# Kernel optimization log

Measured on AMD Instinct MI355X. Metric: run time of the kernel, lower is better.

The kernel has to match this reference:

```python
import jax, jax.numpy as jnp
import numpy as np

N = 40000          # nodes
E = 640000         # edges (before self-loops)
G = 64             # graphs
EMBED_DIM = 128
GAT_HIDDEN = 64    # per-head channels for g1/g2
GAT_OUT_DIM = 64   # per-head channels for g3 (concat=False)
HEADS = (4, 4, 4)
NEG_SLOPE = 0.2


def setup_inputs() -> dict:
    key = jax.random.key(0)
    ks = jax.random.split(key, 16)
    x = jax.random.normal(ks[0], (N, EMBED_DIM), dtype=jnp.float32)
    edge_index = jax.random.randint(ks[1], (2, E), 0, N, dtype=jnp.int64)
    batch = jnp.sort(jax.random.randint(ks[2], (N,), 0, G, dtype=jnp.int64))

    def lin(k, i, o):
        return jax.random.normal(k, (i, o), dtype=jnp.float32) * (1.0 / np.sqrt(i))

    H1, H2, H3 = HEADS
    d1_in, d1_out = EMBED_DIM, GAT_HIDDEN
    d2_in, d2_out = GAT_HIDDEN * H1, GAT_HIDDEN
    d3_in, d3_out = GAT_HIDDEN * H2, GAT_OUT_DIM
    params = dict(
        Wl1=lin(ks[3], d1_in, H1 * d1_out), Wr1=lin(ks[4], d1_in, H1 * d1_out),
        att1=jax.random.normal(ks[5], (H1, d1_out), dtype=jnp.float32) * 0.1,
        b1=jnp.zeros((H1 * d1_out,), jnp.float32),
        Wl2=lin(ks[6], d2_in, H2 * d2_out), Wr2=lin(ks[7], d2_in, H2 * d2_out),
        att2=jax.random.normal(ks[8], (H2, d2_out), dtype=jnp.float32) * 0.1,
        b2=jnp.zeros((H2 * d2_out,), jnp.float32),
        Wl3=lin(ks[9], d3_in, H3 * d3_out), Wr3=lin(ks[10], d3_in, H3 * d3_out),
        att3=jax.random.normal(ks[11], (H3, d3_out), dtype=jnp.float32) * 0.1,
        b3=jnp.zeros((d3_out,), jnp.float32),
        Wc=lin(ks[12], GAT_OUT_DIM, 2), bc=jnp.zeros((2,), jnp.float32),
    )
    return dict(x=x, edge_index=edge_index, batch=batch, **params)


def _gatv2(x, src, dst, Wl, Wr, att, bias, heads, out_c, concat):
    n = x.shape[0]
    xl = (x @ Wl).reshape(n, heads, out_c)   # source transform
    xr = (x @ Wr).reshape(n, heads, out_c)   # target transform
    # per-edge GATv2 score: att . LeakyReLU(xl[j] + xr[i])
    e = jax.nn.leaky_relu(xl[src] + xr[dst], NEG_SLOPE)      # [E,H,C]
    score = jnp.einsum('ehc,hc->eh', e, att)                  # [E,H]
    # segment softmax over incoming edges of each target node
    smax = jax.ops.segment_max(score, dst, num_segments=n)
    escore = jnp.exp(score - smax[dst])
    denom = jax.ops.segment_sum(escore, dst, num_segments=n)
    alpha = escore / (denom[dst] + 1e-16)                     # [E,H]
    out = jax.ops.segment_sum(alpha[:, :, None] * xl[src], dst, num_segments=n)
    out = out.reshape(n, heads * out_c) if concat else out.mean(axis=1)
    return out + bias


def reference(x, edge_index, batch, Wl1, Wr1, att1, b1, Wl2, Wr2, att2, b2,
              Wl3, Wr3, att3, b3, Wc, bc):
    n = x.shape[0]
    loops = jnp.arange(n, dtype=edge_index.dtype)
    src = jnp.concatenate([edge_index[0], loops])  # add self-loops (PyG default)
    dst = jnp.concatenate([edge_index[1], loops])
    act = lambda h: jax.nn.leaky_relu(h, NEG_SLOPE)
    h = act(_gatv2(x, src, dst, Wl1, Wr1, att1, b1, HEADS[0], GAT_HIDDEN, True))
    h = act(_gatv2(h, src, dst, Wl2, Wr2, att2, b2, HEADS[1], GAT_HIDDEN, True))
    h = _gatv2(h, src, dst, Wl3, Wr3, att3, b3, HEADS[2], GAT_OUT_DIM, False)
    g = jax.ops.segment_max(h, batch, num_segments=G)  # global_max_pool
    logits = g @ Wc + bc
    return logits, g
```

## Files before the change

kernel.cpp:

```cpp
#include <hip/hip_runtime.h>
#include <cstdint>

#define NN 40000
#define EE 640000
#define GG 64

typedef short bf16x8 __attribute__((ext_vector_type(8)));
typedef float f32x4 __attribute__((ext_vector_type(4)));

__device__ __forceinline__ float lrelu(float x) { return x > 0.f ? x : 0.2f * x; }

__device__ __forceinline__ unsigned short f2bf(float f) {
    unsigned u = __float_as_uint(f);
    return (unsigned short)((u + 0x7FFFu + ((u >> 16) & 1u)) >> 16);
}
__device__ __forceinline__ float bf2f(unsigned short h) {
    return __uint_as_float(((unsigned)h) << 16);
}

__device__ __forceinline__ unsigned fenc(float x) {
    unsigned u = __float_as_uint(x);
    return (u & 0x80000000u) ? ~u : (u | 0x80000000u);
}
__device__ __forceinline__ float fdec(unsigned e) {
    unsigned u = (e & 0x80000000u) ? (e ^ 0x80000000u) : ~e;
    return __uint_as_float(u);
}
#define ENC_NEG_INF 0x007FFFFFu

__global__ void k_init(int* deg, unsigned* gmax) {
    int i = blockIdx.x * blockDim.x + threadIdx.x;
    if (i < NN) deg[i] = 0;
    if (i < GG * 64) gmax[i] = ENC_NEG_INF;
}

__global__ void k_count(const int* __restrict__ dst, int* deg) {
    int e = blockIdx.x * blockDim.x + threadIdx.x;
    if (e < EE) atomicAdd(&deg[dst[e]], 1);
}

#define SCAN_T 1024
__global__ __launch_bounds__(SCAN_T) void k_scan(const int* __restrict__ deg,
                                                 int* row_ptr, int* cursor) {
    __shared__ int part[SCAN_T];
    const int t = threadIdx.x;
    const int CH = (NN + SCAN_T - 1) / SCAN_T;
    const int base = t * CH;
    int s = 0;
    for (int j = 0; j < CH; ++j) {
        int idx = base + j;
        if (idx < NN) s += deg[idx];
    }
    part[t] = s;
    __syncthreads();
    for (int off = 1; off < SCAN_T; off <<= 1) {
        int v = (t >= off) ? part[t - off] : 0;
        __syncthreads();
        part[t] += v;
        __syncthreads();
    }
    int run = (t == 0) ? 0 : part[t - 1];
    for (int j = 0; j < CH; ++j) {
        int idx = base + j;
        if (idx < NN) {
            row_ptr[idx] = run;
            cursor[idx]  = run;
            run += deg[idx];
        }
    }
    if (t == SCAN_T - 1) row_ptr[NN] = run;
}

__global__ void k_scatter(const int* __restrict__ src, const int* __restrict__ dst,
                          int* cursor, int* csr_src) {
    int e = blockIdx.x * blockDim.x + threadIdx.x;
    if (e < EE) {
        int p = atomicAdd(&cursor[dst[e]], 1);
        csr_src[p] = src[e];
    }
}

__global__ void k_xsplit(const float* __restrict__ x,
                         ushort* __restrict__ ah, ushort* __restrict__ am,
                         ushort* __restrict__ al, int total4) {
    int i = blockIdx.x * blockDim.x + threadIdx.x;
    if (i >= total4) return;
    float4 v = ((const float4*)x)[i];
    ushort4 H, M, L;
    float* pv = &v.x;
    unsigned short* pH = &H.x; unsigned short* pM = &M.x; unsigned short* pL = &L.x;
#pragma unroll
    for (int j = 0; j < 4; ++j) {
        float a = pv[j];
        unsigned short h = f2bf(a);
        float r1 = a - bf2f(h);
        unsigned short m = f2bf(r1);
        float r2 = r1 - bf2f(m);
        unsigned short l = f2bf(r2);
        pH[j] = h; pM[j] = m; pL[j] = l;
    }
    ((ushort4*)ah)[i] = H;
    ((ushort4*)am)[i] = M;
    ((ushort4*)al)[i] = L;
}

__global__ __launch_bounds__(256) void k_wsplit(const float* __restrict__ W, int K,
                                                ushort* __restrict__ th,
                                                ushort* __restrict__ tm,
                                                ushort* __restrict__ tl) {
    __shared__ float t[32][33];
    const int n0 = blockIdx.x * 32;
    const int k0 = blockIdx.y * 32;
    const int tx = threadIdx.x;
    const int ty = threadIdx.y;
#pragma unroll
    for (int i = 0; i < 4; ++i) {
        int kl = ty * 4 + i;
        t[kl][tx] = W[(size_t)(k0 + kl) * 256 + n0 + tx];
    }
    __syncthreads();
#pragma unroll
    for (int i = 0; i < 4; ++i) {
        int nl = ty * 4 + i;
        float a = t[tx][nl];
        unsigned short h = f2bf(a);
        float r1 = a - bf2f(h);
        unsigned short m = f2bf(r1);
        float r2 = r1 - bf2f(m);
        unsigned short l = f2bf(r2);
        size_t o = (size_t)(n0 + nl) * K + k0 + tx;
        th[o] = h; tm[o] = m; tl[o] = l;
    }
}

#define GBM 128
#define GBK 32
__global__ __launch_bounds__(256, 2) void gemm3(const ushort* __restrict__ Ah,
                                                const ushort* __restrict__ Am,
                                                const ushort* __restrict__ Al,
                                                const ushort* __restrict__ Bh,
                                                const ushort* __restrict__ Bm,
                                                const ushort* __restrict__ Bl,
                                                float* __restrict__ C,
                                                int M, int K) {
    __shared__ ushort sA[3][GBM * GBK];
    __shared__ ushort sB[3][GBM * GBK];
    const int tid  = threadIdx.x;
    const int lane = tid & 63;
    const int wv   = tid >> 6;
    const int wm   = wv & 1;
    const int wn   = wv >> 1;
    const int bm   = blockIdx.x * GBM;
    const int bn   = blockIdx.y * 128;

    f32x4 acc[4][4];
#pragma unroll
    for (int i = 0; i < 4; ++i)
#pragma unroll
        for (int j = 0; j < 4; ++j)
            acc[i][j] = (f32x4){0.f, 0.f, 0.f, 0.f};

    const ushort* Aarr[3] = {Ah, Am, Al};
    const ushort* Barr[3] = {Bh, Bm, Bl};

    for (int k0 = 0; k0 < K; k0 += GBK) {
#pragma unroll
        for (int qq = 0; qq < 2; ++qq) {
            const int q   = tid + qq * 256;
            const int row = q >> 2;
            const int c   = q & 3;
            const int cs  = c ^ ((row >> 1) & 3);
            const int lidx = row * 32 + cs * 8;
            int ga = bm + row; if (ga >= M) ga = M - 1;
            const size_t aoff = (size_t)ga * K + k0 + c * 8;
            const size_t boff = (size_t)(bn + row) * K + k0 + c * 8;
#pragma unroll
            for (int s = 0; s < 3; ++s) {
                *(uint4*)&sA[s][lidx] = *(const uint4*)&Aarr[s][aoff];
                *(uint4*)&sB[s][lidx] = *(const uint4*)&Barr[s][boff];
            }
        }
        __syncthreads();

        bf16x8 a[3][4], b[3][4];
        const int fc = lane >> 4;
        const int fr = lane & 15;
#pragma unroll
        for (int mi = 0; mi < 4; ++mi) {
            const int row = wm * 64 + mi * 16 + fr;
            const int cs  = fc ^ ((row >> 1) & 3);
            const int idx = row * 32 + cs * 8;
#pragma unroll
            for (int s = 0; s < 3; ++s)
                a[s][mi] = *(const bf16x8*)&sA[s][idx];
        }
#pragma unroll
        for (int ni = 0; ni < 4; ++ni) {
            const int row = wn * 64 + ni * 16 + fr;
            const int cs  = fc ^ ((row >> 1) & 3);
            const int idx = row * 32 + cs * 8;
#pragma unroll
            for (int s = 0; s < 3; ++s)
                b[s][ni] = *(const bf16x8*)&sB[s][idx];
        }

#pragma unroll
        for (int mi = 0; mi < 4; ++mi)
#pragma unroll
            for (int ni = 0; ni < 4; ++ni) {
                f32x4 c0 = acc[mi][ni];
                c0 = __builtin_amdgcn_mfma_f32_16x16x32_bf16(a[0][mi], b[0][ni], c0, 0, 0, 0);
                c0 = __builtin_amdgcn_mfma_f32_16x16x32_bf16(a[0][mi], b[1][ni], c0, 0, 0, 0);
                c0 = __builtin_amdgcn_mfma_f32_16x16x32_bf16(a[1][mi], b[0][ni], c0, 0, 0, 0);
                c0 = __builtin_amdgcn_mfma_f32_16x16x32_bf16(a[0][mi], b[2][ni], c0, 0, 0, 0);
                c0 = __builtin_amdgcn_mfma_f32_16x16x32_bf16(a[2][mi], b[0][ni], c0, 0, 0, 0);
                c0 = __builtin_amdgcn_mfma_f32_16x16x32_bf16(a[1][mi], b[1][ni], c0, 0, 0, 0);
                acc[mi][ni] = c0;
            }
        __syncthreads();
    }

#pragma unroll
    for (int mi = 0; mi < 4; ++mi) {
#pragma unroll
        for (int r = 0; r < 4; ++r) {
            const int row = bm + wm * 64 + mi * 16 + (lane >> 4) * 4 + r;
            if (row < M) {
#pragma unroll
                for (int ni = 0; ni < 4; ++ni) {
                    const int col = bn + wn * 64 + ni * 16 + (lane & 15);
                    C[(size_t)row * 256 + col] = acc[mi][ni][r];
                }
            }
        }
    }
}

template <int MODE>
__global__ __launch_bounds__(256) void k_aggregate(const float* __restrict__ xl,
                                                   const float* __restrict__ xr,
                                                   const float* __restrict__ att,
                                                   const float* __restrict__ bias,
                                                   const int* __restrict__ row_ptr,
                                                   const int* __restrict__ csr_src,
                                                   ushort* __restrict__ oh,
                                                   ushort* __restrict__ om,
                                                   ushort* __restrict__ ol,
                                                   float* __restrict__ of) {
    const int wave = threadIdx.x >> 6;
    const int lane = threadIdx.x & 63;
    const int node = blockIdx.x * 4 + wave;
    if (node >= NN) return;

    const float4 xri = ((const float4*)(xr + (size_t)node * 256))[lane];
    const float4 av  = ((const float4*)att)[lane];

    float m = -INFINITY, d = 0.f;
    float acc0 = 0.f, acc1 = 0.f, acc2 = 0.f, acc3 = 0.f;

    const int start = row_ptr[node];
    const int end   = row_ptr[node + 1];
    const int L = end - start + 1;

    int i = 0;
    for (; i + 1 < L; i += 2) {
        const int ea = start + i, eb = start + i + 1;
        const int sa = (ea < end) ? csr_src[ea] : node;
        const int sb = (eb < end) ? csr_src[eb] : node;
        const float4 xa = ((const float4*)(xl + (size_t)sa * 256))[lane];
        const float4 xb = ((const float4*)(xl + (size_t)sb * 256))[lane];
        float pa = av.x * lrelu(xa.x + xri.x) + av.y * lrelu(xa.y + xri.y)
                 + av.z * lrelu(xa.z + xri.z) + av.w * lrelu(xa.w + xri.w);
        float pb = av.x * lrelu(xb.x + xri.x) + av.y * lrelu(xb.y + xri.y)
                 + av.z * lrelu(xb.z + xri.z) + av.w * lrelu(xb.w + xri.w);
        pa += __shfl_xor(pa, 1); pb += __shfl_xor(pb, 1);
        pa += __shfl_xor(pa, 2); pb += __shfl_xor(pb, 2);
        pa += __shfl_xor(pa, 4); pb += __shfl_xor(pb, 4);
        pa += __shfl_xor(pa, 8); pb += __shfl_xor(pb, 8);

        const float mn    = fmaxf(m, fmaxf(pa, pb));
        const float scale = __expf(m - mn);
        const float fa    = __expf(pa - mn);
        const float fb    = __expf(pb - mn);
        d    = d * scale + fa + fb;
        acc0 = acc0 * scale + fa * xa.x + fb * xb.x;
        acc1 = acc1 * scale + fa * xa.y + fb * xb.y;
        acc2 = acc2 * scale + fa * xa.z + fb * xb.z;
        acc3 = acc3 * scale + fa * xa.w + fb * xb.w;
        m = mn;
    }
    if (i < L) {
        const int ea = start + i;
        const int sa = (ea < end) ? csr_src[ea] : node;
        const float4 xa = ((const float4*)(xl + (size_t)sa * 256))[lane];
        float pa = av.x * lrelu(xa.x + xri.x) + av.y * lrelu(xa.y + xri.y)
                 + av.z * lrelu(xa.z + xri.z) + av.w * lrelu(xa.w + xri.w);
        pa += __shfl_xor(pa, 1);
        pa += __shfl_xor(pa, 2);
        pa += __shfl_xor(pa, 4);
        pa += __shfl_xor(pa, 8);
        const float mn    = fmaxf(m, pa);
        const float scale = __expf(m - mn);
        const float fa    = __expf(pa - mn);
        d    = d * scale + fa;
        acc0 = acc0 * scale + fa * xa.x;
        acc1 = acc1 * scale + fa * xa.y;
        acc2 = acc2 * scale + fa * xa.z;
        acc3 = acc3 * scale + fa * xa.w;
        m = mn;
    }

    const float inv = 1.f / (d + 1e-16f);
    if (MODE == 0) {
        const int c = lane * 4;
        float v[4];
        v[0] = lrelu(acc0 * inv + bias[c + 0]);
        v[1] = lrelu(acc1 * inv + bias[c + 1]);
        v[2] = lrelu(acc2 * inv + bias[c + 2]);
        v[3] = lrelu(acc3 * inv + bias[c + 3]);
        ushort4 H, M4, L4;
        unsigned short* pH = &H.x; unsigned short* pM = &M4.x; unsigned short* pL = &L4.x;
#pragma unroll
        for (int j = 0; j < 4; ++j) {
            unsigned short h = f2bf(v[j]);
            float r1 = v[j] - bf2f(h);
            unsigned short mm = f2bf(r1);
            float r2 = r1 - bf2f(mm);
            pH[j] = h; pM[j] = mm; pL[j] = f2bf(r2);
        }
        const size_t o = (size_t)node * 64 + lane;
        ((ushort4*)oh)[o] = H;
        ((ushort4*)om)[o] = M4;
        ((ushort4*)ol)[o] = L4;
    } else {
        float v0 = acc0 * inv, v1 = acc1 * inv, v2 = acc2 * inv, v3 = acc3 * inv;
        v0 += __shfl_xor(v0, 16); v0 += __shfl_xor(v0, 32);
        v1 += __shfl_xor(v1, 16); v1 += __shfl_xor(v1, 32);
        v2 += __shfl_xor(v2, 16); v2 += __shfl_xor(v2, 32);
        v3 += __shfl_xor(v3, 16); v3 += __shfl_xor(v3, 32);
        if (lane < 16) {
            const int c = lane * 4;
            float4 o;
            o.x = v0 * 0.25f + bias[c + 0];
            o.y = v1 * 0.25f + bias[c + 1];
            o.z = v2 * 0.25f + bias[c + 2];
            o.w = v3 * 0.25f + bias[c + 3];
            ((float4*)(of + (size_t)node * 64))[lane] = o;
        }
    }
}

#define PNB 32
__global__ __launch_bounds__(64) void k_pool(const float* __restrict__ h3,
                                             const int* __restrict__ batch,
                                             unsigned* gmax) {
    const int lane = threadIdx.x;
    const int start = blockIdx.x * PNB;
    if (start >= NN) return;
    const int end = min(start + PNB, NN);
    int curg = batch[start];
    float best = -INFINITY;
    for (int n = start; n < end; ++n) {
        int g = batch[n];
        if (g != curg) {
            atomicMax(&gmax[curg * 64 + lane], fenc(best));
            best = -INFINITY;
            curg = g;
        }
        best = fmaxf(best, h3[(size_t)n * 64 + lane]);
    }
    atomicMax(&gmax[curg * 64 + lane], fenc(best));
}

__global__ void k_decode(const unsigned* __restrict__ gmax, float* __restrict__ outg) {
    int i = blockIdx.x * blockDim.x + threadIdx.x;
    if (i < GG * 64) outg[i] = fdec(gmax[i]);
}

__global__ __launch_bounds__(128) void k_head(const float* __restrict__ g,
                                              const float* __restrict__ Wc,
                                              const float* __restrict__ bc,
                                              float* __restrict__ logits) {
    const int t = threadIdx.x;
    const int gr = t >> 1, o = t & 1;
    float s = bc[o];
    for (int c = 0; c < 64; ++c) s = fmaf(g[gr * 64 + c], Wc[c * 2 + o], s);
    logits[t] = s;
}

extern "C" void kernel_launch(void* const* d_in, const int* in_sizes, int n_in,
                              void* d_out, int out_size, void* d_ws, size_t ws_size,
                              hipStream_t stream) {
    const float* x     = (const float*)d_in[0];
    const int*   ei    = (const int*)d_in[1];
    const int*   batch = (const int*)d_in[2];
    const float* Wl1 = (const float*)d_in[3];
    const float* Wr1 = (const float*)d_in[4];
    const float* att1 = (const float*)d_in[5];
    const float* b1  = (const float*)d_in[6];
    const float* Wl2 = (const float*)d_in[7];
    const float* Wr2 = (const float*)d_in[8];
    const float* att2 = (const float*)d_in[9];
    const float* b2  = (const float*)d_in[10];
    const float* Wl3 = (const float*)d_in[11];
    const float* Wr3 = (const float*)d_in[12];
    const float* att3 = (const float*)d_in[13];
    const float* b3  = (const float*)d_in[14];
    const float* Wc  = (const float*)d_in[15];
    const float* bc  = (const float*)d_in[16];
    float* out = (float*)d_out;

    char* ws = (char*)d_ws;
    size_t off = 0;
    auto alloc = [&](size_t bytes) -> void* {
        void* p = ws + off;
        off += (bytes + 255) & ~(size_t)255;
        return p;
    };
    float*  xlout = (float*)alloc((size_t)NN * 256 * 4);
    float*  xrout = (float*)alloc((size_t)NN * 256 * 4);
    ushort* Ah    = (ushort*)alloc((size_t)NN * 256 * 2);
    ushort* Am    = (ushort*)alloc((size_t)NN * 256 * 2);
    ushort* Al    = (ushort*)alloc((size_t)NN * 256 * 2);
    ushort* wt[6][3];
    for (int w = 0; w < 6; ++w)
        for (int s = 0; s < 3; ++s)
            wt[w][s] = (ushort*)alloc((size_t)256 * 256 * 2);
    int*   deg     = (int*)alloc((size_t)NN * 4);
    int*   cursor  = (int*)alloc((size_t)NN * 4);
    int*   row_ptr = (int*)alloc((size_t)(NN + 1) * 4);
    int*   csr_src = (int*)alloc((size_t)EE * 4);
    unsigned* gmax = (unsigned*)alloc((size_t)GG * 64 * 4);
    float* h3 = (float*)Ah;
    if (off > ws_size) return;

    const int* esrc = ei;
    const int* edst = ei + EE;

    k_init<<<(NN + 255) / 256, 256, 0, stream>>>(deg, gmax);
    k_count<<<(EE + 255) / 256, 256, 0, stream>>>(edst, deg);
    k_scan<<<1, SCAN_T, 0, stream>>>(deg, row_ptr, cursor);
    k_scatter<<<(EE + 255) / 256, 256, 0, stream>>>(esrc, edst, cursor, csr_src);

    k_xsplit<<<(NN * 128 / 4 + 255) / 256, 256, 0, stream>>>(x, Ah, Am, Al, NN * 128 / 4);
    const float* Ws[6] = {Wl1, Wr1, Wl2, Wr2, Wl3, Wr3};
    const int    Ks[6] = {128, 128, 256, 256, 256, 256};
    for (int w = 0; w < 6; ++w) {
        dim3 g(8, Ks[w] / 32), b(32, 8);
        k_wsplit<<<g, b, 0, stream>>>(Ws[w], Ks[w], wt[w][0], wt[w][1], wt[w][2]);
    }

    const dim3 gg((NN + GBM - 1) / GBM, 2);
    const int agg_blocks = NN / 4;

    gemm3<<<gg, 256, 0, stream>>>(Ah, Am, Al, wt[0][0], wt[0][1], wt[0][2], xlout, NN, 128);
    gemm3<<<gg, 256, 0, stream>>>(Ah, Am, Al, wt[1][0], wt[1][1], wt[1][2], xrout, NN, 128);
    k_aggregate<0><<<agg_blocks, 256, 0, stream>>>(xlout, xrout, att1, b1, row_ptr, csr_src,
                                                   Ah, Am, Al, nullptr);
    gemm3<<<gg, 256, 0, stream>>>(Ah, Am, Al, wt[2][0], wt[2][1], wt[2][2], xlout, NN, 256);
    gemm3<<<gg, 256, 0, stream>>>(Ah, Am, Al, wt[3][0], wt[3][1], wt[3][2], xrout, NN, 256);
    k_aggregate<0><<<agg_blocks, 256, 0, stream>>>(xlout, xrout, att2, b2, row_ptr, csr_src,
                                                   Ah, Am, Al, nullptr);
    gemm3<<<gg, 256, 0, stream>>>(Ah, Am, Al, wt[4][0], wt[4][1], wt[4][2], xlout, NN, 256);
    gemm3<<<gg, 256, 0, stream>>>(Ah, Am, Al, wt[5][0], wt[5][1], wt[5][2], xrout, NN, 256);
    k_aggregate<1><<<agg_blocks, 256, 0, stream>>>(xlout, xrout, att3, b3, row_ptr, csr_src,
                                                   nullptr, nullptr, nullptr, h3);

    k_pool<<<(NN + PNB - 1) / PNB, 64, 0, stream>>>(h3, batch, gmax);
    k_decode<<<(GG * 64 + 255) / 256, 256, 0, stream>>>(gmax, out + 128);
    k_head<<<1, 128, 0, stream>>>(out + 128, Wc, bc, out);
}
```

Baseline: 805.9 us.

## Use 2-term bf16 split GEMM, direct-to-LDS loads, and lazy-rescale softmax aggregation

The fp32-emulating GEMM drops from a three-way bf16 split (six MFMAs per tile) to a two-way split (three MFMAs), and the low-part arrays, their writes and their storage are removed. Global-to-LDS staging now uses the global_load_lds builtin, with each wave loading one operand. The aggregation loop processes four edges per iteration and skips the online-softmax rescale unless a score exceeds the running max by more than 8. These changes cut GEMM compute and memory traffic, register pressure and exp work, at the cost of lower GEMM precision (about 16 mantissa bits).

```diff
diff --git a/kernel.cpp b/kernel.cpp
--- a/kernel.cpp
+++ b/kernel.cpp
@@ -27,6 +27,13 @@
     return __uint_as_float(u);
 }
 #define ENC_NEG_INF 0x007FFFFFu
+
+__device__ __forceinline__ void gload16(const void* g, void* l) {
+    __builtin_amdgcn_global_load_lds(
+        (const __attribute__((address_space(1))) unsigned int*)g,
+        (__attribute__((address_space(3))) unsigned int*)l,
+        16, 0, 0);
+}
 
 __global__ void k_init(int* deg, unsigned* gmax) {
     int i = blockIdx.x * blockDim.x + threadIdx.x;
@@ -81,33 +88,27 @@
 }
 
 __global__ void k_xsplit(const float* __restrict__ x,
-                         ushort* __restrict__ ah, ushort* __restrict__ am,
-                         ushort* __restrict__ al, int total4) {
+                         ushort* __restrict__ ah, ushort* __restrict__ am, int total4) {
     int i = blockIdx.x * blockDim.x + threadIdx.x;
     if (i >= total4) return;
     float4 v = ((const float4*)x)[i];
-    ushort4 H, M, L;
+    ushort4 H, M;
     float* pv = &v.x;
-    unsigned short* pH = &H.x; unsigned short* pM = &M.x; unsigned short* pL = &L.x;
+    unsigned short* pH = &H.x; unsigned short* pM = &M.x;
 #pragma unroll
     for (int j = 0; j < 4; ++j) {
         float a = pv[j];
         unsigned short h = f2bf(a);
-        float r1 = a - bf2f(h);
-        unsigned short m = f2bf(r1);
-        float r2 = r1 - bf2f(m);
-        unsigned short l = f2bf(r2);
-        pH[j] = h; pM[j] = m; pL[j] = l;
+        pH[j] = h;
+        pM[j] = f2bf(a - bf2f(h));
     }
     ((ushort4*)ah)[i] = H;
     ((ushort4*)am)[i] = M;
-    ((ushort4*)al)[i] = L;
 }
 
 __global__ __launch_bounds__(256) void k_wsplit(const float* __restrict__ W, int K,
                                                 ushort* __restrict__ th,
-                                                ushort* __restrict__ tm,
-                                                ushort* __restrict__ tl) {
+                                                ushort* __restrict__ tm) {
     __shared__ float t[32][33];
     const int n0 = blockIdx.x * 32;
     const int k0 = blockIdx.y * 32;
@@ -124,27 +125,24 @@
         int nl = ty * 4 + i;
         float a = t[tx][nl];
         unsigned short h = f2bf(a);
-        float r1 = a - bf2f(h);
-        unsigned short m = f2bf(r1);
-        float r2 = r1 - bf2f(m);
-        unsigned short l = f2bf(r2);
         size_t o = (size_t)(n0 + nl) * K + k0 + tx;
-        th[o] = h; tm[o] = m; tl[o] = l;
+        th[o] = h;
+        tm[o] = f2bf(a - bf2f(h));
     }
 }
 
 #define GBM 128
 #define GBK 32
-__global__ __launch_bounds__(256, 2) void gemm3(const ushort* __restrict__ Ah,
+__global__ __launch_bounds__(256, 2) void gemm2(const ushort* __restrict__ Ah,
                                                 const ushort* __restrict__ Am,
-                                                const ushort* __restrict__ Al,
                                                 const ushort* __restrict__ Bh,
                                                 const ushort* __restrict__ Bm,
-                                                const ushort* __restrict__ Bl,
                                                 float* __restrict__ C,
                                                 int M, int K) {
-    __shared__ ushort sA[3][GBM * GBK];
-    __shared__ ushort sB[3][GBM * GBK];
+    __shared__ ushort sAh[GBM * GBK];
+    __shared__ ushort sAm[GBM * GBK];
+    __shared__ ushort sBh[GBM * GBK];
+    __shared__ ushort sBm[GBM * GBK];
     const int tid  = threadIdx.x;
     const int lane = tid & 63;
     const int wv   = tid >> 6;
@@ -153,6 +151,10 @@
     const int bm   = blockIdx.x * GBM;
     const int bn   = blockIdx.y * 128;
 
+    const ushort* gsrc = (wv == 0) ? Ah : (wv == 1) ? Am : (wv == 2) ? Bh : Bm;
+    ushort* lbase = (wv == 0) ? sAh : (wv == 1) ? sAm : (wv == 2) ? sBh : sBm;
+    const int rowbase = (wv < 2) ? bm : bn;
+
     f32x4 acc[4][4];
 #pragma unroll
     for (int i = 0; i < 4; ++i)
@@ -160,48 +162,36 @@
         for (int j = 0; j < 4; ++j)
             acc[i][j] = (f32x4){0.f, 0.f, 0.f, 0.f};
 
-    const ushort* Aarr[3] = {Ah, Am, Al};
-    const ushort* Barr[3] = {Bh, Bm, Bl};
+    const int rl = lane >> 2;
+    const int cs = lane & 3;
+    const int fc = lane >> 4;
+    const int fr = lane & 15;
 
     for (int k0 = 0; k0 < K; k0 += GBK) {
 #pragma unroll
-        for (int qq = 0; qq < 2; ++qq) {
-            const int q   = tid + qq * 256;
-            const int row = q >> 2;
-            const int c   = q & 3;
-            const int cs  = c ^ ((row >> 1) & 3);
-            const int lidx = row * 32 + cs * 8;
-            int ga = bm + row; if (ga >= M) ga = M - 1;
-            const size_t aoff = (size_t)ga * K + k0 + c * 8;
-            const size_t boff = (size_t)(bn + row) * K + k0 + c * 8;
-#pragma unroll
-            for (int s = 0; s < 3; ++s) {
-                *(uint4*)&sA[s][lidx] = *(const uint4*)&Aarr[s][aoff];
-                *(uint4*)&sB[s][lidx] = *(const uint4*)&Barr[s][boff];
-            }
+        for (int j = 0; j < 8; ++j) {
+            const int lrow = j * 16 + rl;
+            const int c    = cs ^ ((lrow >> 1) & 3);
+            int grow = rowbase + lrow;
+            grow = (grow >= M) ? (M - 1) : grow;
+            gload16(gsrc + (size_t)grow * K + k0 + c * 8, lbase + j * 512);
         }
         __syncthreads();
 
-        bf16x8 a[3][4], b[3][4];
-        const int fc = lane >> 4;
-        const int fr = lane & 15;
+        bf16x8 aH[4], aM[4], bH[4], bM[4];
 #pragma unroll
         for (int mi = 0; mi < 4; ++mi) {
             const int row = wm * 64 + mi * 16 + fr;
-            const int cs  = fc ^ ((row >> 1) & 3);
-            const int idx = row * 32 + cs * 8;
-#pragma unroll
-            for (int s = 0; s < 3; ++s)
-                a[s][mi] = *(const bf16x8*)&sA[s][idx];
+            const int idx = row * 32 + (fc ^ ((row >> 1) & 3)) * 8;
+            aH[mi] = *(const bf16x8*)&sAh[idx];
+            aM[mi] = *(const bf16x8*)&sAm[idx];
         }
 #pragma unroll
         for (int ni = 0; ni < 4; ++ni) {
             const int row = wn * 64 + ni * 16 + fr;
-            const int cs  = fc ^ ((row >> 1) & 3);
-            const int idx = row * 32 + cs * 8;
-#pragma unroll
-            for (int s = 0; s < 3; ++s)
-                b[s][ni] = *(const bf16x8*)&sB[s][idx];
+            const int idx = row * 32 + (fc ^ ((row >> 1) & 3)) * 8;
+            bH[ni] = *(const bf16x8*)&sBh[idx];
+            bM[ni] = *(const bf16x8*)&sBm[idx];
         }
 
 #pragma unroll
@@ -209,12 +199,9 @@
 #pragma unroll
             for (int ni = 0; ni < 4; ++ni) {
                 f32x4 c0 = acc[mi][ni];
-                c0 = __builtin_amdgcn_mfma_f32_16x16x32_bf16(a[0][mi], b[0][ni], c0, 0, 0, 0);
-                c0 = __builtin_amdgcn_mfma_f32_16x16x32_bf16(a[0][mi], b[1][ni], c0, 0, 0, 0);
-                c0 = __builtin_amdgcn_mfma_f32_16x16x32_bf16(a[1][mi], b[0][ni], c0, 0, 0, 0);
-                c0 = __builtin_amdgcn_mfma_f32_16x16x32_bf16(a[0][mi], b[2][ni], c0, 0, 0, 0);
-                c0 = __builtin_amdgcn_mfma_f32_16x16x32_bf16(a[2][mi], b[0][ni], c0, 0, 0, 0);
-                c0 = __builtin_amdgcn_mfma_f32_16x16x32_bf16(a[1][mi], b[1][ni], c0, 0, 0, 0);
+                c0 = __builtin_amdgcn_mfma_f32_16x16x32_bf16(aH[mi], bH[ni], c0, 0, 0, 0);
+                c0 = __builtin_amdgcn_mfma_f32_16x16x32_bf16(aH[mi], bM[ni], c0, 0, 0, 0);
+                c0 = __builtin_amdgcn_mfma_f32_16x16x32_bf16(aM[mi], bH[ni], c0, 0, 0, 0);
                 acc[mi][ni] = c0;
             }
         __syncthreads();
@@ -245,7 +232,6 @@
                                                    const int* __restrict__ csr_src,
                                                    ushort* __restrict__ oh,
                                                    ushort* __restrict__ om,
-                                                   ushort* __restrict__ ol,
                                                    float* __restrict__ of) {
     const int wave = threadIdx.x >> 6;
     const int lane = threadIdx.x & 63;
@@ -256,84 +242,109 @@
     const float4 av  = ((const float4*)att)[lane];
 
     float m = -INFINITY, d = 0.f;
-    float acc0 = 0.f, acc1 = 0.f, acc2 = 0.f, acc3 = 0.f;
+    float a0 = 0.f, a1 = 0.f, a2 = 0.f, a3 = 0.f;
 
     const int start = row_ptr[node];
-    const int end   = row_ptr[node + 1];
-    const int L = end - start + 1;
+    const int endp  = row_ptr[node + 1];
+    const int L = endp - start + 1;
 
     int i = 0;
-    for (; i + 1 < L; i += 2) {
-        const int ea = start + i, eb = start + i + 1;
-        const int sa = (ea < end) ? csr_src[ea] : node;
-        const int sb = (eb < end) ? csr_src[eb] : node;
-        const float4 xa = ((const float4*)(xl + (size_t)sa * 256))[lane];
-        const float4 xb = ((const float4*)(xl + (size_t)sb * 256))[lane];
-        float pa = av.x * lrelu(xa.x + xri.x) + av.y * lrelu(xa.y + xri.y)
-                 + av.z * lrelu(xa.z + xri.z) + av.w * lrelu(xa.w + xri.w);
-        float pb = av.x * lrelu(xb.x + xri.x) + av.y * lrelu(xb.y + xri.y)
-                 + av.z * lrelu(xb.z + xri.z) + av.w * lrelu(xb.w + xri.w);
-        pa += __shfl_xor(pa, 1); pb += __shfl_xor(pb, 1);
-        pa += __shfl_xor(pa, 2); pb += __shfl_xor(pb, 2);
-        pa += __shfl_xor(pa, 4); pb += __shfl_xor(pb, 4);
-        pa += __shfl_xor(pa, 8); pb += __shfl_xor(pb, 8);
-
-        const float mn    = fmaxf(m, fmaxf(pa, pb));
-        const float scale = __expf(m - mn);
-        const float fa    = __expf(pa - mn);
-        const float fb    = __expf(pb - mn);
-        d    = d * scale + fa + fb;
-        acc0 = acc0 * scale + fa * xa.x + fb * xb.x;
-        acc1 = acc1 * scale + fa * xa.y + fb * xb.y;
-        acc2 = acc2 * scale + fa * xa.z + fb * xb.z;
-        acc3 = acc3 * scale + fa * xa.w + fb * xb.w;
-        m = mn;
-    }
-    if (i < L) {
-        const int ea = start + i;
-        const int sa = (ea < end) ? csr_src[ea] : node;
-        const float4 xa = ((const float4*)(xl + (size_t)sa * 256))[lane];
-        float pa = av.x * lrelu(xa.x + xri.x) + av.y * lrelu(xa.y + xri.y)
-                 + av.z * lrelu(xa.z + xri.z) + av.w * lrelu(xa.w + xri.w);
-        pa += __shfl_xor(pa, 1);
-        pa += __shfl_xor(pa, 2);
-        pa += __shfl_xor(pa, 4);
-        pa += __shfl_xor(pa, 8);
-        const float mn    = fmaxf(m, pa);
-        const float scale = __expf(m - mn);
-        const float fa    = __expf(pa - mn);
-        d    = d * scale + fa;
-        acc0 = acc0 * scale + fa * xa.x;
-        acc1 = acc1 * scale + fa * xa.y;
-        acc2 = acc2 * scale + fa * xa.z;
-        acc3 = acc3 * scale + fa * xa.w;
-        m = mn;
+    for (; i + 4 <= L; i += 4) {
+        const int e0 = start + i;
+        const int s0 = (e0     < endp) ? csr_src[e0]     : node;
+        const int s1 = (e0 + 1 < endp) ? csr_src[e0 + 1] : node;
+        const int s2 = (e0 + 2 < endp) ? csr_src[e0 + 2] : node;
+        const int s3 = (e0 + 3 < endp) ? csr_src[e0 + 3] : node;
+        const float4 x0 = ((const float4*)(xl + (size_t)s0 * 256))[lane];
+        const float4 x1 = ((const float4*)(xl + (size_t)s1 * 256))[lane];
+        const float4 x2 = ((const float4*)(xl + (size_t)s2 * 256))[lane];
+        const float4 x3 = ((const float4*)(xl + (size_t)s3 * 256))[lane];
+        float p0 = av.x * lrelu(x0.x + xri.x) + av.y * lrelu(x0.y + xri.y)
+                 + av.z * lrelu(x0.z + xri.z) + av.w * lrelu(x0.w + xri.w);
+        float p1 = av.x * lrelu(x1.x + xri.x) + av.y * lrelu(x1.y + xri.y)
+                 + av.z * lrelu(x1.z + xri.z) + av.w * lrelu(x1.w + xri.w);
+        float p2 = av.x * lrelu(x2.x + xri.x) + av.y * lrelu(x2.y + xri.y)
+                 + av.z * lrelu(x2.z + xri.z) + av.w * lrelu(x2.w + xri.w);
+        float p3 = av.x * lrelu(x3.x + xri.x) + av.y * lrelu(x3.y + xri.y)
+                 + av.z * lrelu(x3.z + xri.z) + av.w * lrelu(x3.w + xri.w);
+        p0 += __shfl_xor(p0, 1); p1 += __shfl_xor(p1, 1);
+        p2 += __shfl_xor(p2, 1); p3 += __shfl_xor(p3, 1);
+        p0 += __shfl_xor(p0, 2); p1 += __shfl_xor(p1, 2);
+        p2 += __shfl_xor(p2, 2); p3 += __shfl_xor(p3, 2);
+        p0 += __shfl_xor(p0, 4); p1 += __shfl_xor(p1, 4);
+        p2 += __shfl_xor(p2, 4); p3 += __shfl_xor(p3, 4);
+        p0 += __shfl_xor(p0, 8); p1 += __shfl_xor(p1, 8);
+        p2 += __shfl_xor(p2, 8); p3 += __shfl_xor(p3, 8);
+
+        const float pm = fmaxf(fmaxf(p0, p1), fmaxf(p2, p3));
+        if (__all(pm <= m + 8.f)) {
+            const float f0 = __expf(p0 - m), f1 = __expf(p1 - m);
+            const float f2 = __expf(p2 - m), f3 = __expf(p3 - m);
+            d  += f0 + f1 + f2 + f3;
+            a0 += f0 * x0.x + f1 * x1.x + f2 * x2.x + f3 * x3.x;
+            a1 += f0 * x0.y + f1 * x1.y + f2 * x2.y + f3 * x3.y;
+            a2 += f0 * x0.z + f1 * x1.z + f2 * x2.z + f3 * x3.z;
+            a3 += f0 * x0.w + f1 * x1.w + f2 * x2.w + f3 * x3.w;
+        } else {
+            const float mn = fmaxf(m, pm);
+            const float sc = __expf(m - mn);
+            const float f0 = __expf(p0 - mn), f1 = __expf(p1 - mn);
+            const float f2 = __expf(p2 - mn), f3 = __expf(p3 - mn);
+            d  = d  * sc + f0 + f1 + f2 + f3;
+            a0 = a0 * sc + f0 * x0.x + f1 * x1.x + f2 * x2.x + f3 * x3.x;
+            a1 = a1 * sc + f0 * x0.y + f1 * x1.y + f2 * x2.y + f3 * x3.y;
+            a2 = a2 * sc + f0 * x0.z + f1 * x1.z + f2 * x2.z + f3 * x3.z;
+            a3 = a3 * sc + f0 * x0.w + f1 * x1.w + f2 * x2.w + f3 * x3.w;
+            m = mn;
+        }
+    }
+    for (; i < L; ++i) {
+        const int e0 = start + i;
+        const int s0 = (e0 < endp) ? csr_src[e0] : node;
+        const float4 x0 = ((const float4*)(xl + (size_t)s0 * 256))[lane];
+        float p0 = av.x * lrelu(x0.x + xri.x) + av.y * lrelu(x0.y + xri.y)
+                 + av.z * lrelu(x0.z + xri.z) + av.w * lrelu(x0.w + xri.w);
+        p0 += __shfl_xor(p0, 1);
+        p0 += __shfl_xor(p0, 2);
+        p0 += __shfl_xor(p0, 4);
+        p0 += __shfl_xor(p0, 8);
+        if (__all(p0 <= m + 8.f)) {
+            const float f0 = __expf(p0 - m);
+            d += f0; a0 += f0 * x0.x; a1 += f0 * x0.y; a2 += f0 * x0.z; a3 += f0 * x0.w;
+        } else {
+            const float mn = fmaxf(m, p0);
+            const float sc = __expf(m - mn);
+            const float f0 = __expf(p0 - mn);
+            d  = d  * sc + f0;
+            a0 = a0 * sc + f0 * x0.x;
+            a1 = a1 * sc + f0 * x0.y;
+            a2 = a2 * sc + f0 * x0.z;
+            a3 = a3 * sc + f0 * x0.w;
+            m = mn;
+        }
     }
 
     const float inv = 1.f / (d + 1e-16f);
     if (MODE == 0) {
         const int c = lane * 4;
         float v[4];
-        v[0] = lrelu(acc0 * inv + bias[c + 0]);
-        v[1] = lrelu(acc1 * inv + bias[c + 1]);
-        v[2] = lrelu(acc2 * inv + bias[c + 2]);
-        v[3] = lrelu(acc3 * inv + bias[c + 3]);
-        ushort4 H, M4, L4;
-        unsigned short* pH = &H.x; unsigned short* pM = &M4.x; unsigned short* pL = &L4.x;
+        v[0] = lrelu(a0 * inv + bias[c + 0]);
+        v[1] = lrelu(a1 * inv + bias[c + 1]);
+        v[2] = lrelu(a2 * inv + bias[c + 2]);
+        v[3] = lrelu(a3 * inv + bias[c + 3]);
+        ushort4 H, M4;
+        unsigned short* pH = &H.x; unsigned short* pM = &M4.x;
 #pragma unroll
         for (int j = 0; j < 4; ++j) {
             unsigned short h = f2bf(v[j]);
-            float r1 = v[j] - bf2f(h);
-            unsigned short mm = f2bf(r1);
-            float r2 = r1 - bf2f(mm);
-            pH[j] = h; pM[j] = mm; pL[j] = f2bf(r2);
+            pH[j] = h;
+            pM[j] = f2bf(v[j] - bf2f(h));
         }
         const size_t o = (size_t)node * 64 + lane;
         ((ushort4*)oh)[o] = H;
         ((ushort4*)om)[o] = M4;
-        ((ushort4*)ol)[o] = L4;
     } else {
-        float v0 = acc0 * inv, v1 = acc1 * inv, v2 = acc2 * inv, v3 = acc3 * inv;
+        float v0 = a0 * inv, v1 = a1 * inv, v2 = a2 * inv, v3 = a3 * inv;
         v0 += __shfl_xor(v0, 16); v0 += __shfl_xor(v0, 32);
         v1 += __shfl_xor(v1, 16); v1 += __shfl_xor(v1, 32);
         v2 += __shfl_xor(v2, 16); v2 += __shfl_xor(v2, 32);
@@ -421,10 +432,9 @@
     float*  xrout = (float*)alloc((size_t)NN * 256 * 4);
     ushort* Ah    = (ushort*)alloc((size_t)NN * 256 * 2);
     ushort* Am    = (ushort*)alloc((size_t)NN * 256 * 2);
-    ushort* Al    = (ushort*)alloc((size_t)NN * 256 * 2);
-    ushort* wt[6][3];
+    ushort* wt[6][2];
     for (int w = 0; w < 6; ++w)
-        for (int s = 0; s < 3; ++s)
+        for (int s = 0; s < 2; ++s)
             wt[w][s] = (ushort*)alloc((size_t)256 * 256 * 2);
     int*   deg     = (int*)alloc((size_t)NN * 4);
     int*   cursor  = (int*)alloc((size_t)NN * 4);
@@ -442,29 +452,29 @@
     k_scan<<<1, SCAN_T, 0, stream>>>(deg, row_ptr, cursor);
     k_scatter<<<(EE + 255) / 256, 256, 0, stream>>>(esrc, edst, cursor, csr_src);
 
-    k_xsplit<<<(NN * 128 / 4 + 255) / 256, 256, 0, stream>>>(x, Ah, Am, Al, NN * 128 / 4);
+    k_xsplit<<<(NN * 128 / 4 + 255) / 256, 256, 0, stream>>>(x, Ah, Am, NN * 128 / 4);
     const float* Ws[6] = {Wl1, Wr1, Wl2, Wr2, Wl3, Wr3};
     const int    Ks[6] = {128, 128, 256, 256, 256, 256};
     for (int w = 0; w < 6; ++w) {
         dim3 g(8, Ks[w] / 32), b(32, 8);
-        k_wsplit<<<g, b, 0, stream>>>(Ws[w], Ks[w], wt[w][0], wt[w][1], wt[w][2]);
+        k_wsplit<<<g, b, 0, stream>>>(Ws[w], Ks[w], wt[w][0], wt[w][1]);
     }
 
     const dim3 gg((NN + GBM - 1) / GBM, 2);
     const int agg_blocks = NN / 4;
 
-    gemm3<<<gg, 256, 0, stream>>>(Ah, Am, Al, wt[0][0], wt[0][1], wt[0][2], xlout, NN, 128);
-    gemm3<<<gg, 256, 0, stream>>>(Ah, Am, Al, wt[1][0], wt[1][1], wt[1][2], xrout, NN, 128);
+    gemm2<<<gg, 256, 0, stream>>>(Ah, Am, wt[0][0], wt[0][1], xlout, NN, 128);
+    gemm2<<<gg, 256, 0, stream>>>(Ah, Am, wt[1][0], wt[1][1], xrout, NN, 128);
     k_aggregate<0><<<agg_blocks, 256, 0, stream>>>(xlout, xrout, att1, b1, row_ptr, csr_src,
-                                                   Ah, Am, Al, nullptr);
-    gemm3<<<gg, 256, 0, stream>>>(Ah, Am, Al, wt[2][0], wt[2][1], wt[2][2], xlout, NN, 256);
-    gemm3<<<gg, 256, 0, stream>>>(Ah, Am, Al, wt[3][0], wt[3][1], wt[3][2], xrout, NN, 256);
+                                                   Ah, Am, nullptr);
+    gemm2<<<gg, 256, 0, stream>>>(Ah, Am, wt[2][0], wt[2][1], xlout, NN, 256);
+    gemm2<<<gg, 256, 0, stream>>>(Ah, Am, wt[3][0], wt[3][1], xrout, NN, 256);
     k_aggregate<0><<<agg_blocks, 256, 0, stream>>>(xlout, xrout, att2, b2, row_ptr, csr_src,
-                                                   Ah, Am, Al, nullptr);
-    gemm3<<<gg, 256, 0, stream>>>(Ah, Am, Al, wt[4][0], wt[4][1], wt[4][2], xlout, NN, 256);
-    gemm3<<<gg, 256, 0, stream>>>(Ah, Am, Al, wt[5][0], wt[5][1], wt[5][2], xrout, NN, 256);
+                                                   Ah, Am, nullptr);
+    gemm2<<<gg, 256, 0, stream>>>(Ah, Am, wt[4][0], wt[4][1], xlout, NN, 256);
+    gemm2<<<gg, 256, 0, stream>>>(Ah, Am, wt[5][0], wt[5][1], xrout, NN, 256);
     k_aggregate<1><<<agg_blocks, 256, 0, stream>>>(xlout, xrout, att3, b3, row_ptr, csr_src,
-                                                   nullptr, nullptr, nullptr, h3);
+                                                   nullptr, nullptr, h3);
 
     k_pool<<<(NN + PNB - 1) / PNB, 64, 0, stream>>>(h3, batch, gmax);
     k_decode<<<(GG * 64 + 255) / 256, 256, 0, stream>>>(gmax, out + 128);
```

New measurement: 721.2 us. 1.12x faster.
